# Kernel optimization log

Measured on AMD Instinct MI355X. Metric: run time of the kernel, lower is better.

Reference implementation:

```python
import jax, jax.numpy as jnp
import numpy as np

NEG = -9.0e15
D = 768


def _init_params(key, d):
    ks = jax.random.split(key, 12)
    s = 0.02
    p = {}
    p['Wa'] = jax.random.normal(ks[0], (d, 1), jnp.float32) * s
    p['ba'] = jnp.zeros((1,), jnp.float32)
    for i, name in enumerate(['qs', 'ks', 'qc', 'kc', 'qr', 'kr']):
        p['W' + name] = jax.random.normal(ks[1 + i], (d, d), jnp.float32) * s
        p['b' + name] = jnp.zeros((d,), jnp.float32)
    p['Wf1'] = jax.random.normal(ks[8], (3 * d, d), jnp.float32) * s
    p['bf1'] = jnp.zeros((d,), jnp.float32)
    p['Wf2'] = jax.random.normal(ks[9], (d, d), jnp.float32) * s
    p['bf2'] = jnp.zeros((d,), jnp.float32)
    p['gamma'] = jnp.ones((d,), jnp.float32)
    p['beta'] = jnp.zeros((d,), jnp.float32)
    return p


def setup_inputs() -> dict:
    key = jax.random.key(0)
    k1, k2, k3 = jax.random.split(key, 3)
    B, L = 8, 1024
    inp = {
        'x': jax.random.normal(k1, (B, L, D), jnp.float32),
        'x_ids': jax.random.randint(k2, (B, L), 0, 1000, jnp.int64 if jax.config.read('jax_enable_x64') else jnp.int32).astype(jnp.int32),
        'pad_idx': 0,
    }
    inp.update(_init_params(k3, D))
    return inp


def _forward(x, x_ids, pad_idx, Wa, ba, Wqs, bqs, Wks, bks, Wqc, bqc, Wkc, bkc,
             Wqr, bqr, Wkr, bkr, Wf1, bf1, Wf2, bf2, gamma, beta):
    B, L, d = x.shape
    valid = x_ids != pad_idx                             # [B,L]
    valid_len = valid.sum(axis=1)
    sep_pos = jnp.clip(valid_len // 2, 1, max(1, L - 2))  # [B]
    pos = jnp.arange(L)[None, :]                          # [1,L]
    false_mask = (pos < sep_pos[:, None]) & valid         # [B,L]
    option_mask = (pos > sep_pos[:, None]) & valid        # [B,L]

    # anomaly gate over false segment
    a_logits = (x @ Wa + ba)[..., 0]                      # [B,L]
    a_logits = jnp.where(false_mask, a_logits, NEG)
    gate = jax.nn.softmax(a_logits, axis=1) * false_mask.astype(x.dtype)
    gate = gate / jnp.clip(gate.sum(axis=1, keepdims=True), 1e-8)

    scale = 1.0 / jnp.sqrt(jnp.asarray(d, x.dtype))
    q_sup, k_sup = x @ Wqs + bqs, x @ Wks + bks
    q_con, k_con = x @ Wqc + bqc, x @ Wkc + bkc
    q_rep, k_rep = x @ Wqr + bqr, x @ Wkr + bkr

    sup_s = jnp.einsum('bld,bmd->blm', q_sup, k_sup) * scale
    con_s = jnp.einsum('bld,bmd->blm', q_con, k_con) * scale
    rep_s = jnp.einsum('bld,bmd->blm', q_rep, k_rep) * scale

    pair_mask = false_mask[:, :, None] & option_mask[:, None, :]  # [B,L,L]
    sup_attn = jax.nn.softmax(jnp.where(pair_mask, sup_s, NEG), axis=-1)
    rep_attn = jax.nn.softmax(jnp.where(pair_mask, rep_s + jnp.tanh(con_s), NEG), axis=-1)

    rep_vec = jnp.einsum('blm,bmd->bld', rep_attn, x)
    sup_vec = jnp.einsum('blm,bmd->bld', sup_attn, x)

    anomaly_false = jnp.einsum('bl,bld->bd', gate, x)
    w_rep = jnp.einsum('bl,bld->bd', gate, rep_vec)
    w_sup = jnp.einsum('bl,bld->bd', gate, sup_vec)

    fused = jnp.concatenate([anomaly_false, w_rep, w_sup], axis=-1)
    fused = jnp.maximum(fused @ Wf1 + bf1, 0.0) @ Wf2 + bf2  # dropout = eval identity

    mu = fused.mean(axis=-1, keepdims=True)
    var = ((fused - mu) ** 2).mean(axis=-1, keepdims=True)
    fused = (fused - mu) / jnp.sqrt(var + 1e-5) * gamma + beta
    return fused


def reference(x, x_ids, pad_idx, Wa, ba, Wqs, bqs, Wks, bks, Wqc, bqc, Wkc, bkc,
              Wqr, bqr, Wkr, bkr, Wf1, bf1, Wf2, bf2, gamma, beta):
    return _forward(x, x_ids, pad_idx, Wa, ba, Wqs, bqs, Wks, bks, Wqc, bqc,
                    Wkc, bkc, Wqr, bqr, Wkr, bkr, Wf1, bf1, Wf2, bf2, gamma, beta)
```

## Files before the change

### kernel.cpp

```cpp
#include <hip/hip_runtime.h>
#include <math.h>

#define L 1024
#define NB 8
#define D 768
#define NEGV (-9.0e15f)
#define SCALE 0.036084391824351615f

typedef unsigned short u16;
typedef __attribute__((ext_vector_type(8))) short short8;
typedef __attribute__((ext_vector_type(4))) float float4v;
#define MFMA_BF16 __builtin_amdgcn_mfma_f32_16x16x32_bf16

__device__ __forceinline__ float b2f(u16 u) {
    union { unsigned int i; float f; } v; v.i = ((unsigned int)u) << 16; return v.f;
}
__device__ __forceinline__ u16 f2b(float f) {
    union { float fv; unsigned int i; } v; v.fv = f;
    unsigned int x = v.i;
    x += 0x7fffu + ((x >> 16) & 1u);
    return (u16)(x >> 16);
}

template<int F32>
__device__ __forceinline__ float4 ld4(const void* p, size_t idx) {
    if (F32) return *(const float4*)((const float*)p + idx);
    ushort4 v = *(const ushort4*)((const u16*)p + idx);
    return make_float4(b2f(v.x), b2f(v.y), b2f(v.z), b2f(v.w));
}
template<int F32>
__device__ __forceinline__ float ld1(const void* p, size_t idx) {
    if (F32) return ((const float*)p)[idx];
    return b2f(((const u16*)p)[idx]);
}
__device__ __forceinline__ int ldid(const int* p, size_t idx, int is64) {
    return is64 ? p[idx * 2] : p[idx];
}

__device__ __forceinline__ void detect2(const void* x, const void* ids, int* sh) {
    int tid = threadIdx.x;
    if (tid < 64) {
        u16 u = ((const u16*)x)[tid * 2];
        int e = (u >> 7) & 0xFF;
        unsigned long long balf = __ballot(e >= 100 && e <= 140);
        int v = ((const int*)ids)[tid * 2 + 1];
        unsigned long long bali = __ballot(v != 0);
        if (tid == 0) {
            sh[0] = (__popcll(balf) < 32) ? 1 : 0;
            sh[1] = (bali == 0ULL) ? 1 : 0;
        }
    }
    __syncthreads();
}

#define WS_FLAG  ((size_t)0)
#define WS_SEP   ((size_t)64)
#define WS_C0    ((size_t)128)
#define WS_Z0    ((size_t)192)
#define WS_W1    ((size_t)9472)
#define WS_GATE  ((size_t)18752)
#define WS_CSUP  ((size_t)51520)
#define WS_CREP  ((size_t)84288)
#define WS_AF    ((size_t)117056)
#define WS_WREP  ((size_t)141632)
#define WS_WSUP  ((size_t)166208)
#define WS_HACC  ((size_t)190784)
#define WS_ALOG  ((size_t)215360)
#define WS_T     ((size_t)248128)
#define WS_OACC  ((size_t)303104)
#define WS_XB    ((size_t)524288)
#define WS_Z     ((size_t)13107200)
#define WS_SSUP  ((size_t)31981568)
#define WS_WB    WS_SSUP
#define WS_SCMB  ((size_t)40370176)
#define WS_M     WS_SCMB

struct PP { const void* W[6]; const void* b[6]; };

template<int F32> __device__ void kbias_body(const void* W, const void* vec,
        float* out, float* vs, int xi) {
    int tid = threadIdx.x;
    for (int i = tid; i < D; i += 256) vs[i] = ld1<F32>(vec, i);
    __syncthreads();
    int row = xi * 64 + (tid >> 2);
    int sub = tid & 3;
    float acc = 0.f;
    for (int i = 0; i < 48; ++i) {
        int k = i * 16 + sub * 4;
        float4 wv = ld4<F32>(W, (size_t)row * D + k);
        acc += wv.x * vs[k] + wv.y * vs[k + 1] + wv.z * vs[k + 2] + wv.w * vs[k + 3];
    }
    acc += __shfl_xor(acc, 1);
    acc += __shfl_xor(acc, 2);
    if (sub == 0) out[row] = acc;
}
template<int F32> __device__ void kc0_body(const void* bq, const void* bk,
        float* c0, float* red) {
    int tid = threadIdx.x;
    float s = 0.f;
    for (int i = tid; i < D; i += 256) s += ld1<F32>(bq, i) * ld1<F32>(bk, i);
    red[tid] = s; __syncthreads();
    for (int st = 128; st > 0; st >>= 1) { if (tid < st) red[tid] += red[tid + st]; __syncthreads(); }
    if (tid == 0) c0[0] = red[0];
}

template<int F32> __device__ void kx_body(const void* x, const void* Wa,
        const void* ba, u16* xb, float* alog, float* ws2) {
    int tid = threadIdx.x;
    for (int i = tid; i < D; i += 256) ws2[i] = ld1<F32>(Wa, i);
    __syncthreads();
    int row = blockIdx.x * 32 + (tid >> 3);
    int sub = tid & 7;
    float a0 = 0.f;
    for (int i = 0; i < 24; ++i) {
        int k = i * 32 + sub * 4;
        float4 xv = ld4<F32>(x, (size_t)row * D + k);
        ushort4 o;
        o.x = f2b(xv.x); o.y = f2b(xv.y); o.z = f2b(xv.z); o.w = f2b(xv.w);
        *(ushort4*)(xb + (size_t)row * D + k) = o;
        a0 += xv.x * ws2[k] + xv.y * ws2[k + 1] + xv.z * ws2[k + 2] + xv.w * ws2[k + 3];
    }
    #pragma unroll
    for (int d = 1; d < 8; d <<= 1) a0 += __shfl_xor(a0, d);
    if (sub == 0) alog[row] = a0 + ld1<F32>(ba, 0);
}
__global__ __launch_bounds__(256) void kx(const void* x, const int* ids, PP pp,
        const void* Wa, const void* ba, u16* xb, u16* Wb, float* alog,
        float* z0, float* w1, float* c0f) {
    __shared__ float sf[2 * D];
    __shared__ int fsh[2];
    detect2(x, ids, fsh);
    int F32 = fsh[0];
    int bid = blockIdx.x;
    if (bid < 256) {
        if (F32) kx_body<1>(x, Wa, ba, xb, alog, sf);
        else     kx_body<0>(x, Wa, ba, xb, alog, sf);
        return;
    }
    if (bid < 1984) {
        int t = (bid - 256) / 288, inner = (bid - 256) % 288;
        const void* src = pp.W[t];
        u16* dst = Wb + (size_t)t * D * D;
        size_t base = ((size_t)inner * 256 + threadIdx.x) * 8;
        if (F32) {
            float4 a = *(const float4*)((const float*)src + base);
            float4 b = *(const float4*)((const float*)src + base + 4);
            uint4 o; u16* po = (u16*)&o;
            po[0] = f2b(a.x); po[1] = f2b(a.y); po[2] = f2b(a.z); po[3] = f2b(a.w);
            po[4] = f2b(b.x); po[5] = f2b(b.y); po[6] = f2b(b.z); po[7] = f2b(b.w);
            *(uint4*)(dst + base) = o;
        } else {
            *(uint4*)(dst + base) = *(const uint4*)((const u16*)src + base);
        }
        return;
    }
    int i = bid - 1984;
    int y = i / 12, xi = i % 12;
    float* vs = sf;
    float* red = sf + D;
    if (y == 4) {
        if (xi != 0) return;
        if (F32) kc0_body<1>(pp.b[2], pp.b[3], c0f, red);
        else     kc0_body<0>(pp.b[2], pp.b[3], c0f, red);
        return;
    }
    const void* W; const void* vec; float* out;
    if (y < 3) { W = pp.W[2 * y + 1]; vec = pp.b[2 * y]; out = z0 + y * D; }
    else       { W = pp.W[2];         vec = pp.b[3];     out = w1; }
    if (F32) kbias_body<1>(W, vec, out, vs, xi);
    else     kbias_body<0>(W, vec, out, vs, xi);
}

__device__ __forceinline__ void stage128_async(const u16* __restrict__ G, size_t ld,
        int r0, int k0, u16* S, int tid) {
    int rowa = tid >> 2;
    int koa = ((tid & 3) ^ (rowa & 3)) << 3;
    int wave = tid >> 6;
    const u16* g1 = &G[(size_t)(r0 + rowa) * ld + k0 + koa];
    const u16* g2 = &G[(size_t)(r0 + rowa + 64) * ld + k0 + koa];
    __builtin_amdgcn_global_load_lds((__attribute__((address_space(1))) void*)(u16*)g1,
        (__attribute__((address_space(3))) void*)(S + wave * 512), 16, 0, 0);
    __builtin_amdgcn_global_load_lds((__attribute__((address_space(1))) void*)(u16*)g2,
        (__attribute__((address_space(3))) void*)(S + 2048 + wave * 512), 16, 0, 0);
}
__device__ __forceinline__ void stage64_async(const u16* __restrict__ G, size_t ld,
        int r0, int k0, u16* S, int tid) {
    int rowa = tid >> 2;
    int koa = ((tid & 3) ^ (rowa & 3)) << 3;
    int wave = tid >> 6;
    const u16* g = &G[(size_t)(r0 + rowa) * ld + k0 + koa];
    __builtin_amdgcn_global_load_lds((__attribute__((address_space(1))) void*)(u16*)g,
        (__attribute__((address_space(3))) void*)(S + wave * 512), 16, 0, 0);
}


__device__ __forceinline__ void gemm64_cnt(const u16* __restrict__ A, size_t lda, int r0,
        const u16* __restrict__ B, size_t ldb, int c0,
        u16* As, u16* Bs, float4v acc[2][4]) {
    int tid = threadIdx.x;
    int lane = tid & 63, wave = tid >> 6;
    int wm = (wave >> 1) << 5, wn = (wave & 1) << 6;
    int quad = lane >> 4, lrow = lane & 15;
    int sq = ((quad ^ (lrow & 3)) << 3);
    #pragma unroll
    for (int i = 0; i < 2; ++i)
        #pragma unroll
        for (int j = 0; j < 4; ++j) acc[i][j] = (float4v){0.f, 0.f, 0.f, 0.f};
    stage64_async(A, lda, r0, 0, As, tid);
    stage64_async(A, lda, r0, 32, As + 2048, tid);
    stage128_async(B, ldb, c0, 0, Bs, tid);
    stage128_async(B, ldb, c0, 32, Bs + 4096, tid);
    stage64_async(A, lda, r0, 64, As + 4096, tid);
    stage64_async(A, lda, r0, 96, As + 6144, tid);
    stage128_async(B, ldb, c0, 64, Bs + 8192, tid);
    stage128_async(B, ldb, c0, 96, Bs + 12288, tid);
    #pragma unroll 1
    for (int t = 0; t < 12; ++t) {
        int cur = t & 1;
        if (t != 11) asm volatile("s_waitcnt vmcnt(6)" ::: "memory");
        else         asm volatile("s_waitcnt vmcnt(0)" ::: "memory");
        __builtin_amdgcn_s_barrier();
        const u16* Ab = As + cur * 4096;
        const u16* Bb = Bs + cur * 8192;
        short8 fa[2][2], fb[2][4];
        #pragma unroll
        for (int p = 0; p < 2; ++p) {
            #pragma unroll
            for (int i = 0; i < 2; ++i)
                fa[p][i] = *(const short8*)&Ab[p * 2048 + (wm + i * 16 + lrow) * 32 + sq];
            #pragma unroll
            for (int j = 0; j < 4; ++j)
                fb[p][j] = *(const short8*)&Bb[p * 4096 + (wn + j * 16 + lrow) * 32 + sq];
        }
        asm volatile("s_waitcnt lgkmcnt(0)" ::: "memory");
        __builtin_amdgcn_sched_barrier(0);
        __builtin_amdgcn_s_barrier();
        if (t < 10) {
            int k0 = (t + 2) << 6;
            u16* Ad = As + cur * 4096;
            u16* Bd = Bs + cur * 8192;
            stage64_async(A, lda, r0, k0, Ad, tid);
            stage64_async(A, lda, r0, k0 + 32, Ad + 2048, tid);
            stage128_async(B, ldb, c0, k0, Bd, tid);
            stage128_async(B, ldb, c0, k0 + 32, Bd + 4096, tid);
        }
        #pragma unroll
        for (int p = 0; p < 2; ++p)
            #pragma unroll
            for (int i = 0; i < 2; ++i)
                #pragma unroll
                for (int j = 0; j < 4; ++j)
                    acc[i][j] = MFMA_BF16(fa[p][i], fb[p][j], acc[i][j], 0, 0, 0);
    }
}

__device__ __forceinline__ void gemm128_cnt(const u16* __restrict__ A, size_t lda, int r0,
        const u16* __restrict__ B, size_t ldb, int c0,
        u16* As, u16* Bs, float4v acc[4][4]) {
    int tid = threadIdx.x;
    int lane = tid & 63, wave = tid >> 6;
    int wm = (wave >> 1) << 6, wn = (wave & 1) << 6;
    int quad = lane >> 4, lrow = lane & 15;
    int sq = ((quad ^ (lrow & 3)) << 3);
    #pragma unroll
    for (int i = 0; i < 4; ++i)
        #pragma unroll
        for (int j = 0; j < 4; ++j) acc[i][j] = (float4v){0.f, 0.f, 0.f, 0.f};
    stage128_async(A, lda, r0, 0, As, tid);
    stage128_async(A, lda, r0, 32, As + 4096, tid);
    stage128_async(B, ldb, c0, 0, Bs, tid);
    stage128_async(B, ldb, c0, 32, Bs + 4096, tid);
    stage128_async(A, lda, r0, 64, As + 8192, tid);
    stage128_async(A, lda, r0, 96, As + 12288, tid);
    stage128_async(B, ldb, c0, 64, Bs + 8192, tid);
    stage128_async(B, ldb, c0, 96, Bs + 12288, tid);
    #pragma unroll 1
    for (int t = 0; t < 12; ++t) {
        int cur = t & 1;
        if (t != 11) asm volatile("s_waitcnt vmcnt(8)" ::: "memory");
        else         asm volatile("s_waitcnt vmcnt(0)" ::: "memory");
        __builtin_amdgcn_s_barrier();
        const u16* Ab = As + cur * 8192;
        const u16* Bb = Bs + cur * 8192;
        short8 fa[2][4], fb[2][4];
        #pragma unroll
        for (int p = 0; p < 2; ++p) {
            #pragma unroll
            for (int i = 0; i < 4; ++i)
                fa[p][i] = *(const short8*)&Ab[p * 4096 + (wm + i * 16 + lrow) * 32 + sq];
            #pragma unroll
            for (int j = 0; j < 4; ++j)
                fb[p][j] = *(const short8*)&Bb[p * 4096 + (wn + j * 16 + lrow) * 32 + sq];
        }
        asm volatile("s_waitcnt lgkmcnt(0)" ::: "memory");
        __builtin_amdgcn_sched_barrier(0);
        __builtin_amdgcn_s_barrier();
        if (t < 10) {
            int k0 = (t + 2) << 6;
            u16* Ad = As + cur * 8192;
            u16* Bd = Bs + cur * 8192;
            stage128_async(A, lda, r0, k0, Ad, tid);
            stage128_async(A, lda, r0, k0 + 32, Ad + 4096, tid);
            stage128_async(B, ldb, c0, k0, Bd, tid);
            stage128_async(B, ldb, c0, k0 + 32, Bd + 4096, tid);
        }
        #pragma unroll
        for (int p = 0; p < 2; ++p)
            #pragma unroll
            for (int i = 0; i < 4; ++i)
                #pragma unroll
                for (int j = 0; j < 4; ++j)
                    acc[i][j] = MFMA_BF16(fa[p][i], fb[p][j], acc[i][j], 0, 0, 0);
    }
}

__global__ __launch_bounds__(256) void kB(const void* x, const int* __restrict__ ids,
        const int* __restrict__ padp, const float* __restrict__ alog,
        float* __restrict__ gate, int* __restrict__ sepArr,
        float* __restrict__ af, float* __restrict__ wrep, float* __restrict__ wsup,
        float* __restrict__ hacc, float* __restrict__ oacc,
        float* __restrict__ csup, float* __restrict__ crep,
        const u16* __restrict__ xb, const float* __restrict__ w1,
        const float* __restrict__ c0f, float* __restrict__ tbuf,
        const u16* __restrict__ Wb, u16* __restrict__ Mt) {
    __shared__ __align__(16) u16 SMEM[24576];
    int bid = blockIdx.x;
    int tid = threadIdx.x;
    if (bid >= 8 && bid < 224) {
        int i = bid - 8;
        int p = i / 72, j = i % 72;
        int r0 = (j / 6) * 64, c0m = (j % 6) * 128;
        u16* As = SMEM;
        u16* Bs = SMEM + 8192;
        float4v acc[2][4];
        gemm64_cnt(Wb + (size_t)(2 * p + 1) * D * D, D, r0,
                   Wb + (size_t)(2 * p) * D * D, D, c0m, As, Bs, acc);
        int lane = tid & 63, wave = tid >> 6;
        int wm = (wave >> 1) << 5, wn = (wave & 1) << 6;
        int quad = lane >> 4, lrow = lane & 15;
        u16* out = Mt + (size_t)p * D * D;
        #pragma unroll
        for (int ii = 0; ii < 2; ++ii)
            #pragma unroll
            for (int jj = 0; jj < 4; ++jj) {
                int brow = r0 + wm + ii * 16 + quad * 4;
                int col = c0m + wn + jj * 16 + lrow;
                #pragma unroll
                for (int r = 0; r < 4; ++r)
                    out[(size_t)(brow + r) * D + col] = f2b(acc[ii][jj][r]);
            }
        return;
    }
    if (bid >= 224) {
        int i = bid - 224;
        int b = i >> 2, q = i & 3;
        float* w1s = (float*)SMEM;
        for (int j = tid; j < D; j += 256) w1s[j] = w1[j];
        __syncthreads();
        float c0v = c0f[0];
        int sub = tid & 15;
        int rowi = tid >> 4;
        for (int pass = 0; pass < 8; ++pass) {
            int l = q * 128 + pass * 16 + rowi;
            const u16* xr = xb + ((size_t)b * L + l) * D;
            float a = 0.f;
            #pragma unroll
            for (int i2 = 0; i2 < 6; ++i2) {
                int k = i2 * 128 + sub * 8;
                short8 v = *(const short8*)&xr[k];
                #pragma unroll
                for (int e = 0; e < 8; ++e) a += b2f((u16)v[e]) * w1s[k + e];
            }
            #pragma unroll
            for (int d2 = 1; d2 < 16; d2 <<= 1) a += __shfl_xor(a, d2);
            if (sub == 0) tbuf[b * 512 + l] = a + c0v;
        }
        return;
    }
    float* red = (float*)SMEM;
    int*   ish = (int*)(red + 256);
    detect2(x, ids, ish);
    int is64 = ish[1];
    int b = bid;
    int pad = padp[0];
    int cnt = 0;
    for (int l = tid; l < L; l += 256) cnt += (ldid(ids, (size_t)b * L + l, is64) != pad) ? 1 : 0;
    red[tid] = (float)cnt; __syncthreads();
    for (int s = 128; s > 0; s >>= 1) { if (tid < s) red[tid] += red[tid + s]; __syncthreads(); }
    if (tid == 0) {
        int vl = (int)red[0];
        int sep = vl / 2; if (sep < 1) sep = 1; if (sep > L - 2) sep = L - 2;
        ish[2] = sep; sepArr[b] = sep;
    }
    __syncthreads();
    int sep = ish[2];
    float lv[4]; int lidx[4];
    float mx = -3.4e38f;
    for (int u = 0; u < 4; ++u) {
        int l = tid + u * 256; lidx[u] = l;
        bool fm = (l < sep) && (ldid(ids, (size_t)b * L + l, is64) != pad);
        float v = fm ? alog[b * L + l] : NEGV;
        lv[u] = v; mx = fmaxf(mx, v);
    }
    red[tid] = mx; __syncthreads();
    for (int s = 128; s > 0; s >>= 1) { if (tid < s) red[tid] = fmaxf(red[tid], red[tid + s]); __syncthreads(); }
    mx = red[0]; __syncthreads();
    float se = 0.f;
    for (int u = 0; u < 4; ++u) { lv[u] = expf(lv[u] - mx); se += lv[u]; }
    red[tid] = se; __syncthreads();
    for (int s = 128; s > 0; s >>= 1) { if (tid < s) red[tid] += red[tid + s]; __syncthreads(); }
    float den = fmaxf(red[0], 1e-30f); __syncthreads();
    float gs = 0.f; float gv[4];
    for (int u = 0; u < 4; ++u) {
        int l = lidx[u];
        bool fm = (l < sep) && (ldid(ids, (size_t)b * L + l, is64) != pad);
        float p = lv[u] / den;
        gv[u] = fm ? p : 0.f;
        gs += gv[u];
    }
    red[tid] = gs; __syncthreads();
    for (int s = 128; s > 0; s >>= 1) { if (tid < s) red[tid] += red[tid + s]; __syncthreads(); }
    gs = red[0];
    float inv = 1.f / fmaxf(gs, 1e-8f);
    for (int u = 0; u < 4; ++u) gate[b * L + lidx[u]] = gv[u] * inv;
    for (int l = tid; l < L; l += 256) { csup[b * L + l] = 0.f; crep[b * L + l] = 0.f; }
    for (int i = tid; i < D; i += 256) {
        af[b * D + i] = 0.f; wrep[b * D + i] = 0.f; wsup[b * D + i] = 0.f;
        hacc[b * D + i] = 0.f; oacc[b * D + i] = 0.f;
    }
}

__global__ __launch_bounds__(256) void kZ_mfma(const u16* __restrict__ xb,
        const u16* __restrict__ Mt, const float* __restrict__ z0,
        u16* __restrict__ Zbuf, const int* __restrict__ sepArr) {
    __shared__ __align__(16) u16 As[16384];
    __shared__ __align__(16) u16 Bs[16384];
    int z = blockIdx.z;
    int p = z >> 3, b = z & 7;
    int sep = sepArr[b];
    int r0 = blockIdx.y * 128;
    if (r0 >= sep) return;
    int c0 = blockIdx.x * 128;
    float4v acc[4][4];
    gemm128_cnt(xb + (size_t)b * L * D, D, r0,
                Mt + (size_t)p * D * D, D, c0, As, Bs, acc);
    int lane = threadIdx.x & 63, wave = threadIdx.x >> 6;
    int wm = (wave >> 1) << 6, wn = (wave & 1) << 6;
    int quad = lane >> 4, lrow = lane & 15;
    const float* z0p = z0 + p * D;
    u16* out = Zbuf + ((size_t)p * NB + b) * 512 * D;
    #pragma unroll
    for (int i = 0; i < 4; ++i)
        #pragma unroll
        for (int j = 0; j < 4; ++j) {
            int brow = r0 + wm + i * 16 + quad * 4;
            int col = c0 + wn + j * 16 + lrow;
            float zb = z0p[col];
            #pragma unroll
            for (int r = 0; r < 4; ++r)
                out[(size_t)(brow + r) * D + col] = f2b(acc[i][j][r] + zb);
        }
}

__global__ __launch_bounds__(256) void kS_mfma(const u16* __restrict__ Zbuf,
        const u16* __restrict__ xb, const float* __restrict__ tcbuf,
        const int* __restrict__ sepArr, u16* __restrict__ ssup,
        u16* __restrict__ scmb) {
    __shared__ __align__(16) u16 As[12288];
    __shared__ __align__(16) u16 Bs[8192];
    int b = blockIdx.z;
    int sep = sepArr[b];
    int l0 = blockIdx.y * 64;
    if (l0 >= sep) return;
    int m0 = blockIdx.x * 128;
    if (m0 + 127 <= sep) return;
    int tid = threadIdx.x, lane = tid & 63, wave = tid >> 6;
    int quad = lane >> 4, lrow = lane & 15;
    int wm = (wave >> 1) << 5, wn = (wave & 1) << 6;
    int sq = ((quad ^ (lrow & 3)) << 3);
    const u16* A0 = Zbuf + (size_t)b * 512 * D;
    const u16* A1 = Zbuf + ((size_t)1 * NB + b) * 512 * D;
    const u16* A2 = Zbuf + ((size_t)2 * NB + b) * 512 * D;
    const u16* X = xb + (size_t)b * L * D;
    float4v ac[3][2][4];
    #pragma unroll
    for (int m = 0; m < 3; ++m)
        #pragma unroll
        for (int i = 0; i < 2; ++i)
            #pragma unroll
            for (int j = 0; j < 4; ++j) ac[m][i][j] = (float4v){0.f, 0.f, 0.f, 0.f};
    stage64_async(A0, D, l0, 0, As, tid);
    stage64_async(A1, D, l0, 0, As + 2048, tid);
    stage64_async(A2, D, l0, 0, As + 4096, tid);
    stage128_async(X, D, m0, 0, Bs, tid);
    stage64_async(A0, D, l0, 32, As + 6144, tid);
    stage64_async(A1, D, l0, 32, As + 8192, tid);
    stage64_async(A2, D, l0, 32, As + 10240, tid);
    stage128_async(X, D, m0, 32, Bs + 4096, tid);
    #pragma unroll 1
    for (int t = 0; t < 24; ++t) {
        int cur = t & 1;
        if (t != 23) asm volatile("s_waitcnt vmcnt(5)" ::: "memory");
        else         asm volatile("s_waitcnt vmcnt(0)" ::: "memory");
        __builtin_amdgcn_s_barrier();
        const u16* Ab = As + cur * 6144;
        const u16* Bb = Bs + cur * 4096;
        short8 fb[4], fA[3][2];
        #pragma unroll
        for (int j = 0; j < 4; ++j)
            fb[j] = *(const short8*)&Bb[(wn + j * 16 + lrow) * 32 + sq];
        #pragma unroll
        for (int m = 0; m < 3; ++m)
            #pragma unroll
            for (int i = 0; i < 2; ++i)
                fA[m][i] = *(const short8*)&Ab[m * 2048 + (wm + i * 16 + lrow) * 32 + sq];
        asm volatile("s_waitcnt lgkmcnt(0)" ::: "memory");
        __builtin_amdgcn_sched_barrier(0);
        __builtin_amdgcn_s_barrier();
        if (t < 22) {
            int k0 = (t + 2) << 5;
            u16* Ad = As + cur * 6144;
            u16* Bd = Bs + cur * 4096;
            stage64_async(A0, D, l0, k0, Ad, tid);
            stage64_async(A1, D, l0, k0, Ad + 2048, tid);
            stage64_async(A2, D, l0, k0, Ad + 4096, tid);
            stage128_async(X, D, m0, k0, Bd, tid);
        }
        #pragma unroll
        for (int m = 0; m < 3; ++m)
            #pragma unroll
            for (int i = 0; i < 2; ++i)
                #pragma unroll
                for (int j = 0; j < 4; ++j)
                    ac[m][i][j] = MFMA_BF16(fA[m][i], fb[j], ac[m][i][j], 0, 0, 0);
    }
    const float* tc = tcbuf + (size_t)b * 512;
    u16* os = ssup + (size_t)b * 512 * L;
    u16* oc = scmb + (size_t)b * 512 * L;
    #pragma unroll
    for (int i = 0; i < 2; ++i)
        #pragma unroll
        for (int j = 0; j < 4; ++j) {
            int brow = l0 + wm + i * 16 + quad * 4;
            int col = m0 + wn + j * 16 + lrow;
            #pragma unroll
            for (int r = 0; r < 4; ++r) {
                os[(size_t)(brow + r) * L + col] = f2b(ac[0][i][j][r] * SCALE);
                float vv = ac[2][i][j][r] * SCALE
                         + tanhf((ac[1][i][j][r] + tc[brow + r]) * SCALE);
                oc[(size_t)(brow + r) * L + col] = f2b(vv);
            }
        }
}

__global__ __launch_bounds__(256) void k2bc(const void* __restrict__ x,
        const u16* __restrict__ ssup,
        const u16* __restrict__ scmb, const int* __restrict__ ids,
        const int* __restrict__ padp, const int* __restrict__ sepArr,
        const float* __restrict__ gate, float* __restrict__ csup,
        float* __restrict__ crep) {
    __shared__ float colacc[4][2][1024];
    __shared__ int fsh[2];
    detect2(x, ids, fsh);
    int b = blockIdx.y;
    int sep = sepArr[b];
    int l0 = blockIdx.x * 8;
    int tid = threadIdx.x, lane = tid & 63, w = tid >> 6;
    for (int i = tid; i < 4 * 2 * 1024; i += 256) ((float*)colacc)[i] = 0.f;
    __syncthreads();
    if (l0 < sep) {
        int is64 = fsh[1];
        int pad = padp[0];
        unsigned int okmask = 0;
        #pragma unroll
        for (int u = 0; u < 16; ++u) {
            int m = u * 64 + lane;
            bool ok = (m > sep) && (ldid(ids, (size_t)b * L + m, is64) != pad);
            okmask |= (ok ? 1u : 0u) << u;
        }
        for (int t = 0; t < 2; ++t) {
            int l = l0 + w * 2 + t;
            if (l >= sep) continue;
            float g = gate[b * L + l];
            if (g == 0.f) continue;
            const u16* rs = ssup + ((size_t)b * 512 + l) * L;
            const u16* rc = scmb + ((size_t)b * 512 + l) * L;
            float s0[16], s1[16];
            float mx0 = -3.4e38f, mx1 = -3.4e38f;
            #pragma unroll
            for (int u = 0; u < 16; ++u) {
                int m = u * 64 + lane;
                bool ok = (okmask >> u) & 1u;
                s0[u] = ok ? b2f(rs[m]) : NEGV;
                s1[u] = ok ? b2f(rc[m]) : NEGV;
                mx0 = fmaxf(mx0, s0[u]); mx1 = fmaxf(mx1, s1[u]);
            }
            #pragma unroll
            for (int d = 1; d < 64; d <<= 1) {
                mx0 = fmaxf(mx0, __shfl_xor(mx0, d));
                mx1 = fmaxf(mx1, __shfl_xor(mx1, d));
            }
            float e0 = 0.f, e1 = 0.f;
            #pragma unroll
            for (int u = 0; u < 16; ++u) {
                s0[u] = expf(s0[u] - mx0); e0 += s0[u];
                s1[u] = expf(s1[u] - mx1); e1 += s1[u];
            }
            #pragma unroll
            for (int d = 1; d < 64; d <<= 1) {
                e0 += __shfl_xor(e0, d);
                e1 += __shfl_xor(e1, d);
            }
            float i0 = g / fmaxf(e0, 1e-30f), i1 = g / fmaxf(e1, 1e-30f);
            #pragma unroll
            for (int u = 0; u < 16; ++u) {
                int m = u * 64 + lane;
                colacc[w][0][m] += s0[u] * i0;
                colacc[w][1][m] += s1[u] * i1;
            }
        }
    }
    __syncthreads();
    for (int m = tid; m < 1024; m += 256) {
        float a0 = colacc[0][0][m] + colacc[1][0][m] + colacc[2][0][m] + colacc[3][0][m];
        float a1 = colacc[0][1][m] + colacc[1][1][m] + colacc[2][1][m] + colacc[3][1][m];
        if (a0 != 0.f) atomicAdd(&csup[b * L + m], a0);
        if (a1 != 0.f) atomicAdd(&crep[b * L + m], a1);
    }
}

__global__ __launch_bounds__(256) void k3(const u16* __restrict__ xb,
        const float* __restrict__ gate, const float* __restrict__ csup,
        const float* __restrict__ crep, float* __restrict__ af,
        float* __restrict__ wrep, float* __restrict__ wsup) {
    int b = blockIdx.y, c = blockIdx.x;
    int tid = threadIdx.x;
    float a0 = 0.f, a1 = 0.f, a2 = 0.f;
    float r0 = 0.f, r1 = 0.f, r2 = 0.f;
    float q0 = 0.f, q1 = 0.f, q2 = 0.f;
    for (int mm = 0; mm < 16; ++mm) {
        int m = c * 16 + mm;
        float wg = gate[b * L + m], wr = crep[b * L + m], wq = csup[b * L + m];
        if (wg == 0.f && wr == 0.f && wq == 0.f) continue;
        size_t base = ((size_t)b * L + m) * D;
        float x0 = b2f(xb[base + tid]);
        float x1 = b2f(xb[base + tid + 256]);
        float x2 = b2f(xb[base + tid + 512]);
        a0 += wg * x0; a1 += wg * x1; a2 += wg * x2;
        r0 += wr * x0; r1 += wr * x1; r2 += wr * x2;
        q0 += wq * x0; q1 += wq * x1; q2 += wq * x2;
    }
    atomicAdd(&af[b * D + tid], a0); atomicAdd(&af[b * D + tid + 256], a1); atomicAdd(&af[b * D + tid + 512], a2);
    atomicAdd(&wrep[b * D + tid], r0); atomicAdd(&wrep[b * D + tid + 256], r1); atomicAdd(&wrep[b * D + tid + 512], r2);
    atomicAdd(&wsup[b * D + tid], q0); atomicAdd(&wsup[b * D + tid + 256], q1); atomicAdd(&wsup[b * D + tid + 512], q2);
}

template<int F32> __device__ void kh1_body(const float* af, const float* wrep,
        const float* wsup, const void* Wf1, float* hacc, float* fs) {
    int tid = threadIdx.x;
    int c0 = blockIdx.x * 128, k0 = blockIdx.y * 144;
    for (int e = tid; e < 8 * 144; e += 256) {
        int b = e / 144, kk = e - b * 144;
        int k = k0 + kk;
        float v = (k < D) ? af[b * D + k] : (k < 2 * D) ? wrep[b * D + k - D]
                                                        : wsup[b * D + k - 2 * D];
        fs[b * 144 + kk] = v;
    }
    __syncthreads();
    int col = c0 + (tid & 127);
    int kg = tid >> 7;
    float acc[NB];
    #pragma unroll
    for (int b = 0; b < NB; ++b) acc[b] = 0.f;
    #pragma unroll 4
    for (int r = 0; r < 72; ++r) {
        int kk = kg * 72 + r;
        float w = ld1<F32>(Wf1, (size_t)(k0 + kk) * D + col);
        #pragma unroll
        for (int b = 0; b < NB; ++b) acc[b] += fs[b * 144 + kk] * w;
    }
    #pragma unroll
    for (int b = 0; b < NB; ++b) atomicAdd(&hacc[b * D + col], acc[b]);
}
__global__ __launch_bounds__(256) void kh1(const void* x, const int* ids,
        const float* af, const float* wrep,
        const float* wsup, const void* Wf1, float* hacc) {
    __shared__ float fs[8 * 144];
    __shared__ int fsh[2];
    detect2(x, ids, fsh);
    if (fsh[0]) kh1_body<1>(af, wrep, wsup, Wf1, hacc, fs);
    else        kh1_body<0>(af, wrep, wsup, Wf1, hacc, fs);
}

template<int F32> __device__ void kh2_body(const float* hacc, const void* bf1,
        const void* Wf2, float* oacc, float* hsl) {
    int tid = threadIdx.x;
    int c0 = blockIdx.x * 128, k0 = blockIdx.y * 96;
    for (int e = tid; e < 8 * 96; e += 256) {
        int b = e / 96, kk = e - b * 96;
        int k = k0 + kk;
        hsl[b * 96 + kk] = fmaxf(hacc[b * D + k] + ld1<F32>(bf1, k), 0.f);
    }
    __syncthreads();
    int col = c0 + (tid & 127);
    int kg = tid >> 7;
    float acc[NB];
    #pragma unroll
    for (int b = 0; b < NB; ++b) acc[b] = 0.f;
    #pragma unroll 4
    for (int r = 0; r < 48; ++r) {
        int kk = kg * 48 + r;
        float w = ld1<F32>(Wf2, (size_t)(k0 + kk) * D + col);
        #pragma unroll
        for (int b = 0; b < NB; ++b) acc[b] += hsl[b * 96 + kk] * w;
    }
    #pragma unroll
    for (int b = 0; b < NB; ++b) atomicAdd(&oacc[b * D + col], acc[b]);
}
__global__ __launch_bounds__(256) void kh2(const void* x, const int* ids,
        const float* hacc, const void* bf1,
        const void* Wf2, float* oacc) {
    __shared__ float hsl[8 * 96];
    __shared__ int fsh[2];
    detect2(x, ids, fsh);
    if (fsh[0]) kh2_body<1>(hacc, bf1, Wf2, oacc, hsl);
    else        kh2_body<0>(hacc, bf1, Wf2, oacc, hsl);
}

template<int F32> __device__ void kln_body(const float* oacc, const void* bf2,
        const void* gamma, const void* beta, void* out, float* red) {
    int b = blockIdx.x, tid = threadIdx.x;
    float o[3];
    #pragma unroll
    for (int u = 0; u < 3; ++u) {
        int i = tid + u * 256;
        o[u] = oacc[b * D + i] + ld1<F32>(bf2, i);
    }
    red[tid] = o[0] + o[1] + o[2]; __syncthreads();
    for (int s = 128; s > 0; s >>= 1) { if (tid < s) red[tid] += red[tid + s]; __syncthreads(); }
    float mu = red[0] / (float)D; __syncthreads();
    float vs = 0.f;
    #pragma unroll
    for (int u = 0; u < 3; ++u) vs += (o[u] - mu) * (o[u] - mu);
    red[tid] = vs; __syncthreads();
    for (int s = 128; s > 0; s >>= 1) { if (tid < s) red[tid] += red[tid + s]; __syncthreads(); }
    float var = red[0] / (float)D;
    float rstd = 1.0f / sqrtf(var + 1e-5f);
    #pragma unroll
    for (int u = 0; u < 3; ++u) {
        int i = tid + u * 256;
        float v = (o[u] - mu) * rstd * ld1<F32>(gamma, i) + ld1<F32>(beta, i);
        if (F32) ((float*)out)[b * D + i] = v;
        else     ((u16*)out)[b * D + i] = f2b(v);
    }
}
__global__ __launch_bounds__(256) void kln(const void* x, const int* ids,
        const float* oacc, const void* bf2,
        const void* gamma, const void* beta, void* out) {
    __shared__ float red[256];
    __shared__ int fsh[2];
    detect2(x, ids, fsh);
    if (fsh[0]) kln_body<1>(oacc, bf2, gamma, beta, out, red);
    else        kln_body<0>(oacc, bf2, gamma, beta, out, red);
}

extern "C" void kernel_launch(void* const* d_in, const int* in_sizes, int n_in,
                              void* d_out, int out_size, void* d_ws, size_t ws_size,
                              hipStream_t stream) {
    const void* x    = d_in[0];
    const int* ids   = (const int*)d_in[1];
    const int* padp  = (const int*)d_in[2];
    const void* Wa   = d_in[3];
    const void* ba   = d_in[4];
    PP pp;
    pp.W[0] = d_in[5];  pp.b[0] = d_in[6];
    pp.W[1] = d_in[7];  pp.b[1] = d_in[8];
    pp.W[2] = d_in[9];  pp.b[2] = d_in[10];
    pp.W[3] = d_in[11]; pp.b[3] = d_in[12];
    pp.W[4] = d_in[13]; pp.b[4] = d_in[14];
    pp.W[5] = d_in[15]; pp.b[5] = d_in[16];
    const void* Wf1 = d_in[17]; const void* bf1 = d_in[18];
    const void* Wf2 = d_in[19]; const void* bf2 = d_in[20];
    const void* gamma = d_in[21]; const void* beta = d_in[22];

    char* ws = (char*)d_ws;
    int*   sepArr = (int*)(ws + WS_SEP);
    float* c0   = (float*)(ws + WS_C0);
    float* z0   = (float*)(ws + WS_Z0);
    float* w1   = (float*)(ws + WS_W1);
    float* gate = (float*)(ws + WS_GATE);
    float* csup = (float*)(ws + WS_CSUP);
    float* crep = (float*)(ws + WS_CREP);
    float* af   = (float*)(ws + WS_AF);
    float* wrep = (float*)(ws + WS_WREP);
    float* wsup = (float*)(ws + WS_WSUP);
    float* hacc = (float*)(ws + WS_HACC);
    float* oacc = (float*)(ws + WS_OACC);
    float* alog = (float*)(ws + WS_ALOG);
    float* tbuf = (float*)(ws + WS_T);
    u16* xb   = (u16*)(ws + WS_XB);
    u16* Zbuf = (u16*)(ws + WS_Z);
    u16* Wb   = (u16*)(ws + WS_WB);
    u16* Mt   = (u16*)(ws + WS_M);
    u16* ssup = (u16*)(ws + WS_SSUP);
    u16* scmb = (u16*)(ws + WS_SCMB);

    kx<<<dim3(2044), dim3(256), 0, stream>>>(x, ids, pp, Wa, ba, xb, Wb, alog, z0, w1, c0);
    kB<<<dim3(256), dim3(256), 0, stream>>>(x, ids, padp, alog, gate, sepArr,
                                            af, wrep, wsup, hacc, oacc, csup, crep,
                                            xb, w1, c0, tbuf, Wb, Mt);
    kZ_mfma<<<dim3(6, 4, 24), dim3(256), 0, stream>>>(xb, Mt, z0, Zbuf, sepArr);
    kS_mfma<<<dim3(8, 8, NB), dim3(256), 0, stream>>>(Zbuf, xb, tbuf, sepArr, ssup, scmb);
    k2bc<<<dim3(64, NB), dim3(256), 0, stream>>>(x, ssup, scmb, ids, padp, sepArr,
                                                 gate, csup, crep);
    k3<<<dim3(64, NB), dim3(256), 0, stream>>>(xb, gate, csup, crep, af, wrep, wsup);
    kh1<<<dim3(6, 16), dim3(256), 0, stream>>>(x, ids, af, wrep, wsup, Wf1, hacc);
    kh2<<<dim3(6, 8), dim3(256), 0, stream>>>(x, ids, hacc, bf1, Wf2, oacc);
    kln<<<dim3(NB), dim3(256), 0, stream>>>(x, ids, oacc, bf2, gamma, beta, d_out);
}
```

Before: 271.2 us.

## Fuse score GEMM with masked softmax and gate-weighted column reduction

Replaces the separate score GEMM kernel (which wrote bf16 score matrices to global memory) and the softmax/column-accumulation kernel with one kernel. Each block computes 16 query rows against all option columns, keeps the scores packed as bf16 in registers, and does the row max, sum and gate-weighted column sums in place before doing atomic adds. This removes the round trip of the large score buffers and one launch. In exchange the tiles are much smaller (16 rows, a triple-buffered staging loop) and register pressure is higher, so MFMA utilisation and occupancy may drop.

```diff
diff --git a/kernel.cpp b/kernel.cpp
--- a/kernel.cpp
+++ b/kernel.cpp
@@ -20,6 +20,9 @@
     unsigned int x = v.i;
     x += 0x7fffu + ((x >> 16) & 1u);
     return (u16)(x >> 16);
+}
+__device__ __forceinline__ float unpk(unsigned int w, int h) {
+    return b2f((u16)(h ? (w >> 16) : (w & 0xffffu)));
 }
 
 template<int F32>
@@ -70,10 +73,8 @@
 #define WS_OACC  ((size_t)303104)
 #define WS_XB    ((size_t)524288)
 #define WS_Z     ((size_t)13107200)
-#define WS_SSUP  ((size_t)31981568)
-#define WS_WB    WS_SSUP
-#define WS_SCMB  ((size_t)40370176)
-#define WS_M     WS_SCMB
+#define WS_WB    ((size_t)31981568)
+#define WS_M     ((size_t)40370176)
 
 struct PP { const void* W[6]; const void* b[6]; };
 
@@ -192,7 +193,6 @@
     __builtin_amdgcn_global_load_lds((__attribute__((address_space(1))) void*)(u16*)g,
         (__attribute__((address_space(3))) void*)(S + wave * 512), 16, 0, 0);
 }
-
 
 __device__ __forceinline__ void gemm64_cnt(const u16* __restrict__ A, size_t lda, int r0,
         const u16* __restrict__ B, size_t ldb, int c0,
@@ -462,170 +462,209 @@
         }
 }
 
-__global__ __launch_bounds__(256) void kS_mfma(const u16* __restrict__ Zbuf,
+__device__ __forceinline__ void stageS(const u16* __restrict__ A0,
+        const u16* __restrict__ A1, const u16* __restrict__ A2,
+        const u16* __restrict__ X, int l0, int m0, int k0, u16* S, int tid) {
+    #pragma unroll
+    for (int r = 0; r < 3; ++r) {
+        int slot = r * 256 + tid;
+        int cs = slot < 704 ? slot : 703;
+        const u16* g;
+        if (cs < 192) {
+            int m = cs >> 6, w2 = cs & 63, row = w2 >> 2, sub = w2 & 3;
+            int subsw = sub ^ (row & 3);
+            const u16* Am = (m == 0) ? A0 : (m == 1) ? A1 : A2;
+            g = &Am[(size_t)(l0 + row) * D + k0 + subsw * 8];
+        } else {
+            int s2 = cs - 192, row = s2 >> 2, sub = s2 & 3;
+            int subsw = sub ^ (row & 3);
+            g = &X[(size_t)(m0 + row) * D + k0 + subsw * 8];
+        }
+        __builtin_amdgcn_global_load_lds((__attribute__((address_space(1))) void*)(u16*)g,
+            (__attribute__((address_space(3))) void*)(S + ((r * 256 + (tid & 192)) * 8)), 16, 0, 0);
+    }
+}
+
+__global__ __launch_bounds__(256) void kS2(const u16* __restrict__ Zbuf,
         const u16* __restrict__ xb, const float* __restrict__ tcbuf,
-        const int* __restrict__ sepArr, u16* __restrict__ ssup,
-        u16* __restrict__ scmb) {
-    __shared__ __align__(16) u16 As[12288];
-    __shared__ __align__(16) u16 Bs[8192];
-    int b = blockIdx.z;
-    int sep = sepArr[b];
-    int l0 = blockIdx.y * 64;
-    if (l0 >= sep) return;
-    int m0 = blockIdx.x * 128;
-    if (m0 + 127 <= sep) return;
-    int tid = threadIdx.x, lane = tid & 63, wave = tid >> 6;
-    int quad = lane >> 4, lrow = lane & 15;
-    int wm = (wave >> 1) << 5, wn = (wave & 1) << 6;
-    int sq = ((quad ^ (lrow & 3)) << 3);
-    const u16* A0 = Zbuf + (size_t)b * 512 * D;
-    const u16* A1 = Zbuf + ((size_t)1 * NB + b) * 512 * D;
-    const u16* A2 = Zbuf + ((size_t)2 * NB + b) * 512 * D;
-    const u16* X = xb + (size_t)b * L * D;
-    float4v ac[3][2][4];
-    #pragma unroll
-    for (int m = 0; m < 3; ++m)
-        #pragma unroll
-        for (int i = 0; i < 2; ++i)
-            #pragma unroll
-            for (int j = 0; j < 4; ++j) ac[m][i][j] = (float4v){0.f, 0.f, 0.f, 0.f};
-    stage64_async(A0, D, l0, 0, As, tid);
-    stage64_async(A1, D, l0, 0, As + 2048, tid);
-    stage64_async(A2, D, l0, 0, As + 4096, tid);
-    stage128_async(X, D, m0, 0, Bs, tid);
-    stage64_async(A0, D, l0, 32, As + 6144, tid);
-    stage64_async(A1, D, l0, 32, As + 8192, tid);
-    stage64_async(A2, D, l0, 32, As + 10240, tid);
-    stage128_async(X, D, m0, 32, Bs + 4096, tid);
-    #pragma unroll 1
-    for (int t = 0; t < 24; ++t) {
-        int cur = t & 1;
-        if (t != 23) asm volatile("s_waitcnt vmcnt(5)" ::: "memory");
-        else         asm volatile("s_waitcnt vmcnt(0)" ::: "memory");
-        __builtin_amdgcn_s_barrier();
-        const u16* Ab = As + cur * 6144;
-        const u16* Bb = Bs + cur * 4096;
-        short8 fb[4], fA[3][2];
-        #pragma unroll
-        for (int j = 0; j < 4; ++j)
-            fb[j] = *(const short8*)&Bb[(wn + j * 16 + lrow) * 32 + sq];
-        #pragma unroll
-        for (int m = 0; m < 3; ++m)
-            #pragma unroll
-            for (int i = 0; i < 2; ++i)
-                fA[m][i] = *(const short8*)&Ab[m * 2048 + (wm + i * 16 + lrow) * 32 + sq];
-        asm volatile("s_waitcnt lgkmcnt(0)" ::: "memory");
-        __builtin_amdgcn_sched_barrier(0);
-        __builtin_amdgcn_s_barrier();
-        if (t < 22) {
-            int k0 = (t + 2) << 5;
-            u16* Ad = As + cur * 6144;
-            u16* Bd = Bs + cur * 4096;
-            stage64_async(A0, D, l0, k0, Ad, tid);
-            stage64_async(A1, D, l0, k0, Ad + 2048, tid);
-            stage64_async(A2, D, l0, k0, Ad + 4096, tid);
-            stage128_async(X, D, m0, k0, Bd, tid);
-        }
-        #pragma unroll
-        for (int m = 0; m < 3; ++m)
-            #pragma unroll
-            for (int i = 0; i < 2; ++i)
-                #pragma unroll
-                for (int j = 0; j < 4; ++j)
-                    ac[m][i][j] = MFMA_BF16(fA[m][i], fb[j], ac[m][i][j], 0, 0, 0);
-    }
-    const float* tc = tcbuf + (size_t)b * 512;
-    u16* os = ssup + (size_t)b * 512 * L;
-    u16* oc = scmb + (size_t)b * 512 * L;
-    #pragma unroll
-    for (int i = 0; i < 2; ++i)
-        #pragma unroll
-        for (int j = 0; j < 4; ++j) {
-            int brow = l0 + wm + i * 16 + quad * 4;
-            int col = m0 + wn + j * 16 + lrow;
-            #pragma unroll
-            for (int r = 0; r < 4; ++r) {
-                os[(size_t)(brow + r) * L + col] = f2b(ac[0][i][j][r] * SCALE);
-                float vv = ac[2][i][j][r] * SCALE
-                         + tanhf((ac[1][i][j][r] + tc[brow + r]) * SCALE);
-                oc[(size_t)(brow + r) * L + col] = f2b(vv);
-            }
-        }
-}
-
-__global__ __launch_bounds__(256) void k2bc(const void* __restrict__ x,
-        const u16* __restrict__ ssup,
-        const u16* __restrict__ scmb, const int* __restrict__ ids,
-        const int* __restrict__ padp, const int* __restrict__ sepArr,
-        const float* __restrict__ gate, float* __restrict__ csup,
-        float* __restrict__ crep) {
-    __shared__ float colacc[4][2][1024];
-    __shared__ int fsh[2];
-    detect2(x, ids, fsh);
+        const int* __restrict__ sepArr, const int* __restrict__ ids,
+        const int* __restrict__ padp, const float* __restrict__ gate,
+        float* __restrict__ csup, float* __restrict__ crep) {
+    __shared__ __align__(16) u16 STG[18432];
+    __shared__ float redmx[2][4][16];
+    __shared__ float redsm[2][4][16];
+    __shared__ int ish[1];
     int b = blockIdx.y;
     int sep = sepArr[b];
-    int l0 = blockIdx.x * 8;
-    int tid = threadIdx.x, lane = tid & 63, w = tid >> 6;
-    for (int i = tid; i < 4 * 2 * 1024; i += 256) ((float*)colacc)[i] = 0.f;
+    int l0 = blockIdx.x * 16;
+    if (l0 >= sep) return;
+    int tid = threadIdx.x, lane = tid & 63, wave = tid >> 6;
+    int lrow = lane & 15, quad = lane >> 4;
+    if (tid < 64) {
+        int v = ((const int*)ids)[tid * 2 + 1];
+        unsigned long long bali = __ballot(v != 0);
+        if (tid == 0) ish[0] = (bali == 0ULL) ? 1 : 0;
+    }
     __syncthreads();
-    if (l0 < sep) {
-        int is64 = fsh[1];
-        int pad = padp[0];
-        unsigned int okmask = 0;
-        #pragma unroll
-        for (int u = 0; u < 16; ++u) {
-            int m = u * 64 + lane;
+    int is64 = ish[0];
+    int pad = padp[0];
+    int msta = ((sep + 1) >> 7) << 7;
+    int nchunk = (L - msta) >> 7;
+    const u16* A0 = Zbuf + (size_t)b * 512 * D;
+    const u16* A1 = Zbuf + ((size_t)NB + b) * 512 * D;
+    const u16* A2 = Zbuf + ((size_t)2 * NB + b) * 512 * D;
+    const u16* X  = xb + (size_t)b * L * D;
+    float tcv[4], gr[4];
+    #pragma unroll
+    for (int r = 0; r < 4; ++r) {
+        tcv[r] = tcbuf[b * 512 + l0 + quad * 4 + r];
+        gr[r]  = gate[b * L + l0 + quad * 4 + r];
+    }
+    unsigned int pS[8][2][2], pC[8][2][2];
+    int sq8 = ((quad ^ (lrow & 3)) << 3);
+    #pragma unroll
+    for (int c = 0; c < 8; ++c) {
+      if (c < nchunk) {
+        int m0c = msta + c * 128;
+        float4v acc[3][2];
+        #pragma unroll
+        for (int m = 0; m < 3; ++m)
+            #pragma unroll
+            for (int j = 0; j < 2; ++j) acc[m][j] = (float4v){0.f, 0.f, 0.f, 0.f};
+        stageS(A0, A1, A2, X, l0, m0c, 0,  STG, tid);
+        stageS(A0, A1, A2, X, l0, m0c, 32, STG + 6144, tid);
+        stageS(A0, A1, A2, X, l0, m0c, 64, STG + 12288, tid);
+        #pragma unroll 1
+        for (int t = 0; t < 24; ++t) {
+            int cur = t - (t / 3) * 3;
+            if (t < 22)       asm volatile("s_waitcnt vmcnt(6)" ::: "memory");
+            else if (t == 22) asm volatile("s_waitcnt vmcnt(3)" ::: "memory");
+            else              asm volatile("s_waitcnt vmcnt(0)" ::: "memory");
+            __builtin_amdgcn_s_barrier();
+            const u16* Sb = STG + cur * 6144;
+            short8 fA0 = *(const short8*)&Sb[lrow * 32 + sq8];
+            short8 fA1 = *(const short8*)&Sb[512 + lrow * 32 + sq8];
+            short8 fA2 = *(const short8*)&Sb[1024 + lrow * 32 + sq8];
+            int rB = wave * 32 + lrow;
+            short8 fB0 = *(const short8*)&Sb[1536 + rB * 32 + sq8];
+            short8 fB1 = *(const short8*)&Sb[1536 + (rB + 16) * 32 + sq8];
+            asm volatile("s_waitcnt lgkmcnt(0)" ::: "memory");
+            __builtin_amdgcn_sched_barrier(0);
+            __builtin_amdgcn_s_barrier();
+            if (t < 21) stageS(A0, A1, A2, X, l0, m0c, (t + 3) * 32, STG + cur * 6144, tid);
+            acc[0][0] = MFMA_BF16(fA0, fB0, acc[0][0], 0, 0, 0);
+            acc[0][1] = MFMA_BF16(fA0, fB1, acc[0][1], 0, 0, 0);
+            acc[1][0] = MFMA_BF16(fA1, fB0, acc[1][0], 0, 0, 0);
+            acc[1][1] = MFMA_BF16(fA1, fB1, acc[1][1], 0, 0, 0);
+            acc[2][0] = MFMA_BF16(fA2, fB0, acc[2][0], 0, 0, 0);
+            acc[2][1] = MFMA_BF16(fA2, fB1, acc[2][1], 0, 0, 0);
+        }
+        #pragma unroll
+        for (int j = 0; j < 2; ++j) {
+            int m = m0c + wave * 32 + j * 16 + lrow;
             bool ok = (m > sep) && (ldid(ids, (size_t)b * L + m, is64) != pad);
-            okmask |= (ok ? 1u : 0u) << u;
-        }
-        for (int t = 0; t < 2; ++t) {
-            int l = l0 + w * 2 + t;
-            if (l >= sep) continue;
-            float g = gate[b * L + l];
-            if (g == 0.f) continue;
-            const u16* rs = ssup + ((size_t)b * 512 + l) * L;
-            const u16* rc = scmb + ((size_t)b * 512 + l) * L;
-            float s0[16], s1[16];
-            float mx0 = -3.4e38f, mx1 = -3.4e38f;
-            #pragma unroll
-            for (int u = 0; u < 16; ++u) {
-                int m = u * 64 + lane;
-                bool ok = (okmask >> u) & 1u;
-                s0[u] = ok ? b2f(rs[m]) : NEGV;
-                s1[u] = ok ? b2f(rc[m]) : NEGV;
-                mx0 = fmaxf(mx0, s0[u]); mx1 = fmaxf(mx1, s1[u]);
+            float vs[4], vc[4];
+            #pragma unroll
+            for (int r = 0; r < 4; ++r) {
+                vs[r] = ok ? acc[0][j][r] * SCALE : NEGV;
+                vc[r] = ok ? (acc[2][j][r] * SCALE
+                              + tanhf((acc[1][j][r] + tcv[r]) * SCALE)) : NEGV;
             }
-            #pragma unroll
-            for (int d = 1; d < 64; d <<= 1) {
-                mx0 = fmaxf(mx0, __shfl_xor(mx0, d));
-                mx1 = fmaxf(mx1, __shfl_xor(mx1, d));
+            pS[c][j][0] = (unsigned)f2b(vs[0]) | ((unsigned)f2b(vs[1]) << 16);
+            pS[c][j][1] = (unsigned)f2b(vs[2]) | ((unsigned)f2b(vs[3]) << 16);
+            pC[c][j][0] = (unsigned)f2b(vc[0]) | ((unsigned)f2b(vc[1]) << 16);
+            pC[c][j][1] = (unsigned)f2b(vc[2]) | ((unsigned)f2b(vc[3]) << 16);
+        }
+      }
+    }
+    float mxs[4], mxc[4];
+    #pragma unroll
+    for (int r = 0; r < 4; ++r) { mxs[r] = -3.4e38f; mxc[r] = -3.4e38f; }
+    #pragma unroll
+    for (int c = 0; c < 8; ++c) if (c < nchunk)
+        #pragma unroll
+        for (int j = 0; j < 2; ++j)
+            #pragma unroll
+            for (int r = 0; r < 4; ++r) {
+                mxs[r] = fmaxf(mxs[r], unpk(pS[c][j][r >> 1], r & 1));
+                mxc[r] = fmaxf(mxc[r], unpk(pC[c][j][r >> 1], r & 1));
             }
-            float e0 = 0.f, e1 = 0.f;
-            #pragma unroll
-            for (int u = 0; u < 16; ++u) {
-                s0[u] = expf(s0[u] - mx0); e0 += s0[u];
-                s1[u] = expf(s1[u] - mx1); e1 += s1[u];
+    #pragma unroll
+    for (int d = 1; d < 16; d <<= 1)
+        #pragma unroll
+        for (int r = 0; r < 4; ++r) {
+            mxs[r] = fmaxf(mxs[r], __shfl_xor(mxs[r], d));
+            mxc[r] = fmaxf(mxc[r], __shfl_xor(mxc[r], d));
+        }
+    if (lrow == 0)
+        #pragma unroll
+        for (int r = 0; r < 4; ++r) {
+            redmx[0][wave][quad * 4 + r] = mxs[r];
+            redmx[1][wave][quad * 4 + r] = mxc[r];
+        }
+    __syncthreads();
+    #pragma unroll
+    for (int r = 0; r < 4; ++r) {
+        int rr = quad * 4 + r;
+        mxs[r] = fmaxf(fmaxf(redmx[0][0][rr], redmx[0][1][rr]),
+                       fmaxf(redmx[0][2][rr], redmx[0][3][rr]));
+        mxc[r] = fmaxf(fmaxf(redmx[1][0][rr], redmx[1][1][rr]),
+                       fmaxf(redmx[1][2][rr], redmx[1][3][rr]));
+    }
+    float sms[4], smc[4];
+    #pragma unroll
+    for (int r = 0; r < 4; ++r) { sms[r] = 0.f; smc[r] = 0.f; }
+    #pragma unroll
+    for (int c = 0; c < 8; ++c) if (c < nchunk)
+        #pragma unroll
+        for (int j = 0; j < 2; ++j)
+            #pragma unroll
+            for (int r = 0; r < 4; ++r) {
+                sms[r] += expf(unpk(pS[c][j][r >> 1], r & 1) - mxs[r]);
+                smc[r] += expf(unpk(pC[c][j][r >> 1], r & 1) - mxc[r]);
             }
-            #pragma unroll
-            for (int d = 1; d < 64; d <<= 1) {
-                e0 += __shfl_xor(e0, d);
-                e1 += __shfl_xor(e1, d);
+    #pragma unroll
+    for (int d = 1; d < 16; d <<= 1)
+        #pragma unroll
+        for (int r = 0; r < 4; ++r) {
+            sms[r] += __shfl_xor(sms[r], d);
+            smc[r] += __shfl_xor(smc[r], d);
+        }
+    if (lrow == 0)
+        #pragma unroll
+        for (int r = 0; r < 4; ++r) {
+            redsm[0][wave][quad * 4 + r] = sms[r];
+            redsm[1][wave][quad * 4 + r] = smc[r];
+        }
+    __syncthreads();
+    float wgs[4], wgc[4];
+    #pragma unroll
+    for (int r = 0; r < 4; ++r) {
+        int rr = quad * 4 + r;
+        float ds = redsm[0][0][rr] + redsm[0][1][rr] + redsm[0][2][rr] + redsm[0][3][rr];
+        float dc = redsm[1][0][rr] + redsm[1][1][rr] + redsm[1][2][rr] + redsm[1][3][rr];
+        wgs[r] = gr[r] / fmaxf(ds, 1e-30f);
+        wgc[r] = gr[r] / fmaxf(dc, 1e-30f);
+    }
+    #pragma unroll
+    for (int c = 0; c < 8; ++c) if (c < nchunk) {
+        int m0c = msta + c * 128;
+        #pragma unroll
+        for (int j = 0; j < 2; ++j) {
+            float as = 0.f, ar = 0.f;
+            #pragma unroll
+            for (int r = 0; r < 4; ++r) {
+                as += wgs[r] * expf(unpk(pS[c][j][r >> 1], r & 1) - mxs[r]);
+                ar += wgc[r] * expf(unpk(pC[c][j][r >> 1], r & 1) - mxc[r]);
             }
-            float i0 = g / fmaxf(e0, 1e-30f), i1 = g / fmaxf(e1, 1e-30f);
-            #pragma unroll
-            for (int u = 0; u < 16; ++u) {
-                int m = u * 64 + lane;
-                colacc[w][0][m] += s0[u] * i0;
-                colacc[w][1][m] += s1[u] * i1;
+            as += __shfl_xor(as, 16); as += __shfl_xor(as, 32);
+            ar += __shfl_xor(ar, 16); ar += __shfl_xor(ar, 32);
+            if (quad == 0) {
+                int m = m0c + wave * 32 + j * 16 + lrow;
+                atomicAdd(&csup[b * L + m], as);
+                atomicAdd(&crep[b * L + m], ar);
             }
         }
-    }
-    __syncthreads();
-    for (int m = tid; m < 1024; m += 256) {
-        float a0 = colacc[0][0][m] + colacc[1][0][m] + colacc[2][0][m] + colacc[3][0][m];
-        float a1 = colacc[0][1][m] + colacc[1][1][m] + colacc[2][1][m] + colacc[3][1][m];
-        if (a0 != 0.f) atomicAdd(&csup[b * L + m], a0);
-        if (a1 != 0.f) atomicAdd(&crep[b * L + m], a1);
     }
 }
 
@@ -802,17 +841,14 @@
     u16* Zbuf = (u16*)(ws + WS_Z);
     u16* Wb   = (u16*)(ws + WS_WB);
     u16* Mt   = (u16*)(ws + WS_M);
-    u16* ssup = (u16*)(ws + WS_SSUP);
-    u16* scmb = (u16*)(ws + WS_SCMB);
 
     kx<<<dim3(2044), dim3(256), 0, stream>>>(x, ids, pp, Wa, ba, xb, Wb, alog, z0, w1, c0);
     kB<<<dim3(256), dim3(256), 0, stream>>>(x, ids, padp, alog, gate, sepArr,
                                             af, wrep, wsup, hacc, oacc, csup, crep,
                                             xb, w1, c0, tbuf, Wb, Mt);
     kZ_mfma<<<dim3(6, 4, 24), dim3(256), 0, stream>>>(xb, Mt, z0, Zbuf, sepArr);
-    kS_mfma<<<dim3(8, 8, NB), dim3(256), 0, stream>>>(Zbuf, xb, tbuf, sepArr, ssup, scmb);
-    k2bc<<<dim3(64, NB), dim3(256), 0, stream>>>(x, ssup, scmb, ids, padp, sepArr,
-                                                 gate, csup, crep);
+    kS2<<<dim3(32, NB), dim3(256), 0, stream>>>(Zbuf, xb, tbuf, sepArr, ids, padp,
+                                                gate, csup, crep);
     k3<<<dim3(64, NB), dim3(256), 0, stream>>>(xb, gate, csup, crep, af, wrep, wsup);
     kh1<<<dim3(6, 16), dim3(256), 0, stream>>>(x, ids, af, wrep, wsup, Wf1, hacc);
     kh2<<<dim3(6, 8), dim3(256), 0, stream>>>(x, ids, hacc, bf1, Wf2, oacc);
```

New measurement: 266.2 us. About the same (-1.8%).
